# Optimization experiments

Measured on AMD Instinct MI355X. Metric: run time of the kernel, lower is better.

Reference implementation:

```python
import jax, jax.numpy as jnp
import numpy as np


def _cofactor_antieq(M):
    """ith output = M[...,i,0] * (-1)**i * det(M with row i and col 0 deleted).

    M: (..., n, n) -> (..., n). Vectorized form of the original per-row
    jnp.delete + stack + det construction.
    """
    n = M.shape[-1]
    # rows[i] = all row indices except i, shape (n, n-1)
    rows = np.stack([np.delete(np.arange(n), i) for i in range(n)])
    Msub = M[..., 1:]                 # delete first column: (..., n, n-1)
    sub = Msub[..., rows, :]          # delete row i per output: (..., n, n-1, n-1)
    signs = jnp.asarray((-1.0) ** np.arange(n), dtype=M.dtype)
    return M[..., 0] * signs * jnp.linalg.det(sub)


def setup_inputs() -> dict:
    key = jax.random.key(0)
    ks = jax.random.split(key, 6)
    B, NSPIN, NPS, D, NION, DIM = 4096, 2, 16, 256, 8, 3
    eq_inputs = jax.random.normal(ks[0], (B, NSPIN * NPS, D), jnp.float32)
    r_ei = jax.random.normal(ks[1], (B, NSPIN * NPS, NION, DIM), jnp.float32)
    # per-spin linear orbital params (stacked over spin since splits are equal)
    W = jax.random.normal(ks[2], (NSPIN, D, NPS), jnp.float32) / np.sqrt(D)
    b = jax.random.normal(ks[3], (NSPIN, NPS), jnp.float32) * 0.01
    # anisotropic envelope decay matrices A per (spin, ion, orbital), near identity
    env_dim = jax.random.normal(ks[4], (NSPIN, NION, NPS, DIM, DIM), jnp.float32) * 0.1 + jnp.eye(DIM, dtype=jnp.float32)
    # linear combination over ions per (spin, orbital)
    env_ion = jax.random.normal(ks[5], (NSPIN, NION, NPS), jnp.float32) / NION
    return dict(eq_inputs=eq_inputs, r_ei=r_ei, W=W, b=b, env_dim=env_dim, env_ion=env_ion)


def reference(eq_inputs, r_ei, W, b, env_dim, env_ion):
    B = eq_inputs.shape[0]
    nspin, d, nps = W.shape
    nion, dim = r_ei.shape[-2], r_ei.shape[-1]
    # split particles by spin: (B, nspin, nps, ...)
    xs = eq_inputs.reshape(B, nspin, nps, d)
    rs = r_ei.reshape(B, nspin, nps, nion, dim)
    # linear part of orbitals: (B, s, n, o) with n = o = nps (square per spin)
    y = jnp.einsum('bsnd,sdo->bsno', xs, W) + b[:, None, :]
    # anisotropic exponential envelope: exp(-||A (r - R)||), summed over ions
    Ar = jnp.einsum('sioed,bsnid->bsnioe', env_dim, rs)        # (B,s,n,ion,orb,3)
    env = jnp.einsum('bsnio,sio->bsno',
                     jnp.exp(-jnp.linalg.norm(Ar, axis=-1)), env_ion)
    M = y * env                                                 # (B, s, n, n)
    cof = _cofactor_antieq(M)                                   # (B, s, n)
    return cof[..., None]                                       # (B, s, n, 1)
```

## Files before the change

kernel.cpp:

```cpp
#include <hip/hip_runtime.h>
#include <math.h>


__global__ __launch_bounds__(256)
void cof_matrix(const float* __restrict__ eq,
                const float* __restrict__ rei,
                const float* __restrict__ Wm,
                const float* __restrict__ bb,
                const float* __restrict__ edim,
                const float* __restrict__ eion,
                float* __restrict__ ws)
{
  __shared__ __align__(16) float Gl[8 * 6 * 16];
  __shared__ __align__(16) float Xl[4 * 320];

  const int tid   = threadIdx.x;
  const int lane  = tid & 63;
  const int wv    = tid >> 6;
  const int blk   = blockIdx.x;
  const int sp    = blk >> 10;
  const int bbase = (blk & 1023) * 4;

  if (tid < 128) {
    const int i = tid >> 4, o = tid & 15;
    const float* A = edim + (((size_t)sp * 8 + i) * 16 + o) * 9;
    const float a0=A[0],a1=A[1],a2=A[2],a3=A[3],a4=A[4],a5=A[5],a6=A[6],a7=A[7],a8=A[8];
    float* Gp = Gl + i * 96 + o;
    Gp[0]  = a0*a0 + a3*a3 + a6*a6;
    Gp[16] = a1*a1 + a4*a4 + a7*a7;
    Gp[32] = a2*a2 + a5*a5 + a8*a8;
    Gp[48] = 2.f*(a0*a1 + a3*a4 + a6*a7);
    Gp[64] = 2.f*(a0*a2 + a3*a5 + a6*a8);
    Gp[80] = 2.f*(a1*a2 + a4*a5 + a7*a8);
  }
  __syncthreads();

  const int bidx = bbase + wv;
  const int cch  = lane >> 4;
  const int nb   = (lane >> 2) & 3;
  const int ob   = lane & 3;

  const float* xb = eq + ((size_t)bidx * 32 + sp * 16) * 256;
  const float* wb = Wm + (size_t)sp * 4096;

  float acc[4][4] = {{0.f,0.f,0.f,0.f},{0.f,0.f,0.f,0.f},
                     {0.f,0.f,0.f,0.f},{0.f,0.f,0.f,0.f}};

  #pragma unroll
  for (int q = 0; q < 16; ++q) {
    const int dg = q * 16 + cch * 4;
    float xr[4][4], wr4[4][4];
    #pragma unroll
    for (int r = 0; r < 4; ++r) {
      float4 t = *(const float4*)(xb + (4 * nb + r) * 256 + dg);
      xr[r][0]=t.x; xr[r][1]=t.y; xr[r][2]=t.z; xr[r][3]=t.w;
    }
    #pragma unroll
    for (int j = 0; j < 4; ++j) {
      float4 t = *(const float4*)(wb + (dg + j) * 16 + 4 * ob);
      wr4[j][0]=t.x; wr4[j][1]=t.y; wr4[j][2]=t.z; wr4[j][3]=t.w;
    }
    #pragma unroll
    for (int r = 0; r < 4; ++r)
      #pragma unroll
      for (int j = 0; j < 4; ++j)
        #pragma unroll
        for (int c2 = 0; c2 < 4; ++c2)
          acc[r][c2] = fmaf(xr[r][j], wr4[j][c2], acc[r][c2]);
  }

  #pragma unroll
  for (int r = 0; r < 4; ++r)
    #pragma unroll
    for (int c2 = 0; c2 < 4; ++c2) {
      float v = acc[r][c2];
      v += __shfl_xor(v, 16);
      v += __shfl_xor(v, 32);
      acc[r][c2] = v;
    }

  float* Mw = Xl + wv * 320;
  {
    float4 bv = *(const float4*)(bb + sp * 16 + 4 * ob);
    if (lane < 16) {
      #pragma unroll
      for (int r = 0; r < 4; ++r) {
        float4 v = make_float4(acc[r][0] + bv.x, acc[r][1] + bv.y,
                               acc[r][2] + bv.z, acc[r][3] + bv.w);
        *(float4*)(Mw + (4 * nb + r) * 20 + 4 * ob) = v;
      }
    }
  }

  {
    const int n = lane >> 2;
    const float* rp = rei + ((size_t)bidx * 32 + sp * 16 + n) * 24;
    float rv[24];
    #pragma unroll
    for (int t4 = 0; t4 < 6; ++t4) {
      float4 t = *(const float4*)(rp + t4 * 4);
      rv[t4*4+0]=t.x; rv[t4*4+1]=t.y; rv[t4*4+2]=t.z; rv[t4*4+3]=t.w;
    }
    float4 env = make_float4(0.f, 0.f, 0.f, 0.f);
    #pragma unroll
    for (int i = 0; i < 8; ++i) {
      const float r0 = rv[i*3], r1 = rv[i*3+1], r2 = rv[i*3+2];
      const float rr0 = r0*r0, rr1 = r1*r1, rr2 = r2*r2;
      const float rr3 = r0*r1, rr4 = r0*r2, rr5 = r1*r2;
      const float* Gp = Gl + i * 96 + 4 * ob;
      const float4 q00 = *(const float4*)(Gp);
      const float4 q11 = *(const float4*)(Gp + 16);
      const float4 q22 = *(const float4*)(Gp + 32);
      const float4 q01 = *(const float4*)(Gp + 48);
      const float4 q02 = *(const float4*)(Gp + 64);
      const float4 q12 = *(const float4*)(Gp + 80);
      const float4 io  = *(const float4*)(eion + ((size_t)sp * 8 + i) * 16 + 4 * ob);
#define ENVC(c) { float n2 = q00.c*rr0 + q11.c*rr1 + q22.c*rr2 \
                           + q01.c*rr3 + q02.c*rr4 + q12.c*rr5; \
                  n2 = fmaxf(n2, 0.f); \
                  env.c += __expf(-sqrtf(n2)) * io.c; }
      ENVC(x) ENVC(y) ENVC(z) ENVC(w)
#undef ENVC
    }
    const float* mp = Mw + n * 20 + 4 * ob;
    float4 y = *(const float4*)mp;
    const size_t pair = (size_t)bidx * 2 + sp;
    *(float4*)(ws + pair * 256 + n * 16 + 4 * ob) =
        make_float4(y.x * env.x, y.y * env.y, y.z * env.z, y.w * env.w);
  }
}

__global__ __launch_bounds__(64)
void cof_lu(const float* __restrict__ ws,
            float* __restrict__ out)
{
  const int lane = threadIdx.x;
  const int g  = lane >> 4;
  const int r  = lane & 15;
  const int gb = lane & 48;
  const size_t pair = (size_t)blockIdx.x * 4 + g;
  const float* mg = ws + pair * 256;

  float a[16];
  #pragma unroll
  for (int c = 0; c < 16; ++c) a[c] = mg[c * 16 + r];

  float det = 1.0f;
  int sign = 0;
  unsigned retired = 0;
  unsigned pp0 = 0, pp1 = 0;
  int srr = 0;
  float accf = (r == 0) ? 1.0f : 0.0f;
  float acc2 = 0.0f;

  #pragma unroll
  for (int k = 0; k < 16; ++k) {
    const bool act = ((retired >> r) & 1u) == 0u;
    const float av = act ? fabsf(a[k]) : 0.0f;
    unsigned pk = (__float_as_uint(av) & 0xFFFFFFF0u) | (unsigned)r;
    #pragma unroll
    for (int m = 1; m <= 8; m <<= 1) {
      unsigned o2 = __shfl_xor(pk, m);
      pk = (pk > o2) ? pk : o2;
    }
    const int p = (int)(pk & 15u);
    if (k < 8) pp0 |= (unsigned)p << (4 * k);
    else       pp1 |= (unsigned)p << (4 * (k - 8));
    float pv = __shfl(a[k], gb | p);
    if (fabsf(pv) < 1e-30f) pv = (pv < 0.0f) ? -1e-30f : 1e-30f;
    det *= pv;
    retired |= (1u << p);
    sign ^= (int)(__popc((~retired) & ((1u << p) - 1u)) & 1u);
    if (r == p) srr = k;
    const bool upd = act && (r != p);
    float m2 = 0.0f;
    if (upd) { m2 = a[k] / pv; a[k] = m2; }
    #pragma unroll
    for (int c = k + 1; c < 16; ++c) {
      float bcv = __shfl(a[c], gb | p);
      if (upd) a[c] = fmaf(-m2, bcv, a[c]);
    }
    float zk = __shfl(accf, gb | p);
    if (r == p) acc2 = zk;
    if (upd) accf = fmaf(-m2, zk, accf);
  }
  if (sign) det = -det;

  float myx = 0.0f;
  #pragma unroll
  for (int j = 15; j >= 0; --j) {
    float t = acc2 / a[j];
    const int pj = (int)(((j >= 8) ? (pp1 >> (4 * (j - 8)))
                                   : (pp0 >> (4 * j))) & 15u);
    float xj = __shfl(t, gb | pj);
    if (srr < j) acc2 = fmaf(-a[j], xj, acc2);
    if (r == j) myx = xj;
  }

  const float mi0 = mg[r * 16];
  out[pair * 16 + r] = mi0 * det * myx;
}

extern "C" void kernel_launch(void* const* d_in, const int* in_sizes, int n_in,
                              void* d_out, int out_size, void* d_ws, size_t ws_size,
                              hipStream_t stream) {
  (void)in_sizes; (void)n_in; (void)out_size; (void)ws_size;
  const float* eq   = (const float*)d_in[0];
  const float* rei  = (const float*)d_in[1];
  const float* Wm   = (const float*)d_in[2];
  const float* bb   = (const float*)d_in[3];
  const float* edim = (const float*)d_in[4];
  const float* eion = (const float*)d_in[5];
  float* out = (float*)d_out;
  float* ws  = (float*)d_ws;
  hipLaunchKernelGGL(cof_matrix, dim3(2048), dim3(256), 0, stream,
                     eq, rei, Wm, bb, edim, eion, ws);
  hipLaunchKernelGGL(cof_lu, dim3(2048), dim3(64), 0, stream, ws, out);
}
```

Measured before the change: 236.9 us.

## Stage W and X tiles in shared memory with double-buffered swizzled loads

Copies the per-spin W matrix into LDS once per block and streams each wave's 16x256 X slice through two swizzled LDS buffers. Global loads for the next quarter are issued before the current quarter's FMAs, so memory latency overlaps compute. Global reads become fully coalesced rows instead of strided float4 gathers. LDS use rises to about 50KB per block, which can lower occupancy. It also adds syncs-free wave-private buffers that rely on wave-synchronous execution. Reusing xw0 for Mw is safe only because compute on it has finished.

```diff
diff --git a/kernel.cpp b/kernel.cpp
--- a/kernel.cpp
+++ b/kernel.cpp
@@ -11,8 +11,9 @@
                 const float* __restrict__ eion,
                 float* __restrict__ ws)
 {
+  __shared__ __align__(16) float Wp[4096];
   __shared__ __align__(16) float Gl[8 * 6 * 16];
-  __shared__ __align__(16) float Xl[4 * 320];
+  __shared__ __align__(16) float Xs[4][2][1024];
 
   const int tid   = threadIdx.x;
   const int lane  = tid & 63;
@@ -20,6 +21,14 @@
   const int blk   = blockIdx.x;
   const int sp    = blk >> 10;
   const int bbase = (blk & 1023) * 4;
+
+  const float* wb = Wm + (size_t)sp * 4096;
+
+  #pragma unroll
+  for (int t = 0; t < 4; ++t) {
+    const int idx = t * 256 + tid;
+    ((float4*)Wp)[idx] = ((const float4*)wb)[idx];
+  }
 
   if (tid < 128) {
     const int i = tid >> 4, o = tid & 15;
@@ -41,33 +50,72 @@
   const int ob   = lane & 3;
 
   const float* xb = eq + ((size_t)bidx * 32 + sp * 16) * 256;
-  const float* wb = Wm + (size_t)sp * 4096;
+
+  const int srow = lane >> 4;
+  const int schk = lane & 15;
+
+  float* xw0 = &Xs[wv][0][0];
+  float* xw1 = &Xs[wv][1][0];
 
   float acc[4][4] = {{0.f,0.f,0.f,0.f},{0.f,0.f,0.f,0.f},
                      {0.f,0.f,0.f,0.f},{0.f,0.f,0.f,0.f}};
 
-  #pragma unroll
-  for (int q = 0; q < 16; ++q) {
-    const int dg = q * 16 + cch * 4;
-    float xr[4][4], wr4[4][4];
-    #pragma unroll
-    for (int r = 0; r < 4; ++r) {
-      float4 t = *(const float4*)(xb + (4 * nb + r) * 256 + dg);
-      xr[r][0]=t.x; xr[r][1]=t.y; xr[r][2]=t.z; xr[r][3]=t.w;
-    }
-    #pragma unroll
-    for (int j = 0; j < 4; ++j) {
-      float4 t = *(const float4*)(wb + (dg + j) * 16 + 4 * ob);
-      wr4[j][0]=t.x; wr4[j][1]=t.y; wr4[j][2]=t.z; wr4[j][3]=t.w;
-    }
-    #pragma unroll
-    for (int r = 0; r < 4; ++r)
-      #pragma unroll
-      for (int j = 0; j < 4; ++j)
-        #pragma unroll
-        for (int c2 = 0; c2 < 4; ++c2)
-          acc[r][c2] = fmaf(xr[r][j], wr4[j][c2], acc[r][c2]);
-  }
+  float4 sA[4], sB[4];
+
+#define LOADQ(dst, qq)                                                        \
+  _Pragma("unroll")                                                           \
+  for (int t = 0; t < 4; ++t)                                                 \
+    dst[t] = *(const float4*)(xb + (4 * t + srow) * 256 + (qq) * 64 + schk * 4);
+
+#define WRITEQ(buf, src)                                                      \
+  _Pragma("unroll")                                                           \
+  for (int t = 0; t < 4; ++t) {                                               \
+    const int row_ = 4 * t + srow;                                            \
+    *(float4*)((buf) + row_ * 64 + ((schk ^ row_) << 2)) = src[t];            \
+  }
+
+#define COMPQ(buf, qq)                                                        \
+  _Pragma("unroll")                                                           \
+  for (int g = 0; g < 4; ++g) {                                               \
+    const int dg = (qq) * 64 + g * 16 + cch * 4;                              \
+    float xr[4][4], wr4[4][4];                                                \
+    _Pragma("unroll")                                                         \
+    for (int r = 0; r < 4; ++r) {                                             \
+      const int R_ = 4 * nb + r;                                              \
+      float4 t = *(const float4*)((buf) + R_ * 64 +                           \
+                                  (((g * 4 + cch) ^ R_) << 2));               \
+      xr[r][0]=t.x; xr[r][1]=t.y; xr[r][2]=t.z; xr[r][3]=t.w;                 \
+    }                                                                         \
+    _Pragma("unroll")                                                         \
+    for (int j = 0; j < 4; ++j) {                                             \
+      float4 t = *(const float4*)(Wp + (dg + j) * 16 + 4 * ob);               \
+      wr4[j][0]=t.x; wr4[j][1]=t.y; wr4[j][2]=t.z; wr4[j][3]=t.w;             \
+    }                                                                         \
+    _Pragma("unroll")                                                         \
+    for (int r = 0; r < 4; ++r)                                               \
+      _Pragma("unroll")                                                       \
+      for (int j = 0; j < 4; ++j)                                             \
+        _Pragma("unroll")                                                     \
+        for (int c2 = 0; c2 < 4; ++c2)                                        \
+          acc[r][c2] = fmaf(xr[r][j], wr4[j][c2], acc[r][c2]);                \
+  }
+
+  LOADQ(sA, 0)
+  WRITEQ(xw0, sA)
+  LOADQ(sB, 1)
+  COMPQ(xw0, 0)
+  WRITEQ(xw1, sB)
+  LOADQ(sA, 2)
+  COMPQ(xw1, 1)
+  WRITEQ(xw0, sA)
+  LOADQ(sB, 3)
+  COMPQ(xw0, 2)
+  WRITEQ(xw1, sB)
+  COMPQ(xw1, 3)
+
+#undef LOADQ
+#undef WRITEQ
+#undef COMPQ
 
   #pragma unroll
   for (int r = 0; r < 4; ++r)
@@ -79,7 +127,7 @@
       acc[r][c2] = v;
     }
 
-  float* Mw = Xl + wv * 320;
+  float* Mw = xw0;
   {
     float4 bv = *(const float4*)(bb + sp * 16 + 4 * ob);
     if (lane < 16) {
```

New measurement: 224.6 us. 1.05x faster.
